# Optimization experiments

Measured on AMD Instinct MI355X. Metric: run time of the kernel, lower is better.

## Reference

```python
import jax, jax.numpy as jnp
import numpy as np

NORM_EPS = 1e-05

def _quant_input(x):
    # per-token dynamic int8 fake-quant: s = 127 / max(|x|, 1e-5)
    s = 127.0 / jnp.clip(jnp.max(jnp.abs(x), axis=-1, keepdims=True), 1e-05, None)
    return jnp.clip(jnp.round(x * s), -128.0, 127.0) / s

def _rmsnorm(x, w, eps):
    return x * jax.lax.rsqrt(jnp.mean(x * x, axis=-1, keepdims=True) + eps) * w

def setup_inputs() -> dict:
    key = jax.random.key(0)
    k0, k1, k2 = jax.random.split(key, 3)
    dim, hidden = 2048, 5632
    x = jax.random.normal(k0, (4, 2048, dim), dtype=jnp.float32)
    w13 = jax.random.normal(k1, (2 * hidden, dim), dtype=jnp.float32) * 0.02
    w2 = jax.random.normal(k2, (dim, hidden), dtype=jnp.float32) * 0.02
    norm_w = jnp.ones((hidden,), dtype=jnp.float32)
    return {"x": x, "w13": w13, "w2": w2, "norm_w": norm_w}

def reference(x, w13, w2, norm_w):
    # BitLinear w13: quantize input, then linear
    xq = _quant_input(x)
    x13 = jnp.einsum('bsd,fd->bsf', xq, w13)  # [B,S,2H]
    x1, x3 = jnp.split(x13, 2, axis=-1)
    gated = jnp.square(jax.nn.relu(x1)) * x3  # squared-ReLU gating
    inner = _rmsnorm(gated, norm_w, NORM_EPS)
    # BitLinear w2
    iq = _quant_input(inner)
    out = jnp.einsum('bsh,dh->bsd', iq, w2)
    return out
```

## Files before the change

### kernel.cpp

```cpp
#include <hip/hip_runtime.h>

typedef unsigned short u16;
typedef __attribute__((ext_vector_type(8))) short short8;
typedef __attribute__((ext_vector_type(4))) float f32x4;
typedef __attribute__((ext_vector_type(4))) u16 ushort4v;
typedef __attribute__((ext_vector_type(8))) u16 ushort8v;

#define DIM 2048
#define HID 5632
#define F2  11264
#define TTOT 8192

#define GLD(g, l) __builtin_amdgcn_global_load_lds(                       \
    (const __attribute__((address_space(1))) void*)(g),                   \
    (__attribute__((address_space(3))) void*)(l), 16, 0, 0)

__device__ __forceinline__ u16 f2bf(float f) {
  unsigned int u = __builtin_bit_cast(unsigned int, f);
  u += 0x7FFFu + ((u >> 16) & 1u);
  return (u16)(u >> 16);
}

__global__ __launch_bounds__(256) void conv_w13(const float* __restrict__ w,
                                                u16* __restrict__ o) {
  int idx = blockIdx.x * 256 + threadIdx.x;
  int rnew = idx >> 9;
  int dc = (idx & 511) << 2;
  int b = rnew >> 5, ii = rnew & 31;
  int orig = (ii < 16) ? (b * 16 + ii) : (HID + b * 16 + (ii - 16));
  float4 v = *reinterpret_cast<const float4*>(w + (size_t)orig * DIM + dc);
  ushort4v q = {f2bf(v.x), f2bf(v.y), f2bf(v.z), f2bf(v.w)};
  *reinterpret_cast<ushort4v*>(o + (size_t)rnew * DIM + dc) = q;
}

__global__ __launch_bounds__(256) void conv_w2(const float* __restrict__ w,
                                               u16* __restrict__ o) {
  size_t e = ((size_t)blockIdx.x * 256 + threadIdx.x) * 4;
  float4 v = *reinterpret_cast<const float4*>(w + e);
  ushort4v q = {f2bf(v.x), f2bf(v.y), f2bf(v.z), f2bf(v.w)};
  *reinterpret_cast<ushort4v*>(o + e) = q;
}

__global__ __launch_bounds__(256) void quant_x(const float* __restrict__ x,
                                               u16* __restrict__ q,
                                               float* __restrict__ scale) {
  const int t = blockIdx.x;
  const float* xr = x + (size_t)t * DIM;
  const int tid = threadIdx.x;
  float4 a = *reinterpret_cast<const float4*>(xr + tid * 8);
  float4 b = *reinterpret_cast<const float4*>(xr + tid * 8 + 4);
  float v[8] = {a.x, a.y, a.z, a.w, b.x, b.y, b.z, b.w};
  float m = 0.f;
#pragma unroll
  for (int i = 0; i < 8; ++i) m = fmaxf(m, fabsf(v[i]));
#pragma unroll
  for (int off = 32; off; off >>= 1) m = fmaxf(m, __shfl_xor(m, off));
  __shared__ float red[4];
  if ((tid & 63) == 0) red[tid >> 6] = m;
  __syncthreads();
  m = fmaxf(fmaxf(red[0], red[1]), fmaxf(red[2], red[3]));
  m = fmaxf(m, 1e-5f);
  float s = 127.0f / m;
  if (tid == 0) scale[t] = m / 127.0f;
  ushort8v o;
#pragma unroll
  for (int i = 0; i < 8; ++i) {
    float r = fminf(fmaxf(rintf(v[i] * s), -128.f), 127.f);
    o[i] = f2bf(r);
  }
  *reinterpret_cast<ushort8v*>(q + (size_t)t * DIM + tid * 8) = o;
}

__global__ __launch_bounds__(256) void gate_nq(const float* __restrict__ G,
                                               const float* __restrict__ nw,
                                               u16* __restrict__ q2,
                                               float* __restrict__ s2) {
  const int t = blockIdx.x;
  const float* gr = G + (size_t)t * HID;
  const int tid = threadIdx.x;
  float4 vv[6];
  float ss = 0.f, mx = 0.f;
#pragma unroll
  for (int k = 0; k < 6; ++k) {
    int i = tid + k * 256;
    if (i < 1408) {
      float4 v = *reinterpret_cast<const float4*>(gr + i * 4);
      float4 w4 = *reinterpret_cast<const float4*>(nw + i * 4);
      vv[k] = v;
      ss += v.x * v.x + v.y * v.y + v.z * v.z + v.w * v.w;
      mx = fmaxf(mx, fmaxf(fmaxf(fabsf(v.x * w4.x), fabsf(v.y * w4.y)),
                           fmaxf(fabsf(v.z * w4.z), fabsf(v.w * w4.w))));
    }
  }
#pragma unroll
  for (int off = 32; off; off >>= 1) {
    ss += __shfl_xor(ss, off);
    mx = fmaxf(mx, __shfl_xor(mx, off));
  }
  __shared__ float rs[4], rm[4];
  if ((tid & 63) == 0) { rs[tid >> 6] = ss; rm[tid >> 6] = mx; }
  __syncthreads();
  ss = rs[0] + rs[1] + rs[2] + rs[3];
  mx = fmaxf(fmaxf(rm[0], rm[1]), fmaxf(rm[2], rm[3]));
  float rinv = 1.0f / sqrtf(ss * (1.0f / 5632.0f) + 1e-5f);
  float mi = fmaxf(mx * rinv, 1e-5f);
  float s = 127.0f / mi;
  if (tid == 0) s2[t] = mi / 127.0f;
  float fs = rinv * s;
#pragma unroll
  for (int k = 0; k < 6; ++k) {
    int i = tid + k * 256;
    if (i < 1408) {
      float4 v = vv[k];
      float4 w4 = *reinterpret_cast<const float4*>(nw + i * 4);
      ushort4v o;
      o.x = f2bf(fminf(fmaxf(rintf(v.x * w4.x * fs), -128.f), 127.f));
      o.y = f2bf(fminf(fmaxf(rintf(v.y * w4.y * fs), -128.f), 127.f));
      o.z = f2bf(fminf(fmaxf(rintf(v.z * w4.z * fs), -128.f), 127.f));
      o.w = f2bf(fminf(fmaxf(rintf(v.w * w4.w * fs), -128.f), 127.f));
      *reinterpret_cast<ushort4v*>(q2 + (size_t)t * HID + i * 4) = o;
    }
  }
}

template <int GATE>
__global__ __launch_bounds__(512, 2) void gemm8(
    const u16* __restrict__ A, const u16* __restrict__ B,
    const float* __restrict__ rowscale, float* __restrict__ C,
    int N, int K, int Ntiles) {
  __shared__ __attribute__((aligned(16))) u16 lds[2][2][2][256 * 32];
  const int NT = K >> 6;
  const int nwg = gridDim.x;
  const int orig = blockIdx.x;
  const int qq = nwg >> 3, rr = nwg & 7, xcd = orig & 7, sidx = orig >> 3;
  const int wg = (xcd < rr ? xcd * (qq + 1) : rr * (qq + 1) + (xcd - rr) * qq) + sidx;
  const int mt = wg / Ntiles, nt = wg % Ntiles;

  const int tid = threadIdx.x;
  const int wid = tid >> 6, lane = tid & 63;
  const int wm = wid >> 2, wn = wid & 3;
  const int c16 = lane & 15, q4 = lane >> 4;
  const int rA_base = wm * 128 + c16;
  const int rB_base = wn * 64 + c16;
  const int caf = (q4 ^ ((lane >> 1) & 3)) << 3;

  const int sr = tid >> 2;
  const int scol = ((tid & 3) ^ ((tid >> 3) & 3)) << 3;
  const u16* Ar = A + ((size_t)mt * 256 + sr) * K + scol;
  const u16* Br = B + ((size_t)nt * 256 + sr) * K + scol;
  const size_t rstep = (size_t)128 * K;

  f32x4 acc[8][4];
#pragma unroll
  for (int m = 0; m < 8; ++m)
#pragma unroll
    for (int n = 0; n < 4; ++n) acc[m][n] = f32x4{0.f, 0.f, 0.f, 0.f};

  auto stage = [&](int mat, int kk, int t) {
    if (t < NT) {
      const u16* g = (mat ? Br : Ar) + t * 64 + kk * 32;
      u16* l = &lds[t & 1][mat][kk][wid << 9];
      GLD(g, l);
      GLD(g + rstep, l + 4096);
    }
  };
  auto ldA = [&](int db, int kk, int mh, short8* af) {
#pragma unroll
    for (int m = 0; m < 4; ++m)
      af[m] = *reinterpret_cast<const short8*>(
          &lds[db][0][kk][(rA_base + (mh * 4 + m) * 16) * 32 + caf]);
  };
  auto ldB = [&](int db, int kk, short8* bfr) {
#pragma unroll
    for (int n = 0; n < 4; ++n)
      bfr[n] = *reinterpret_cast<const short8*>(
          &lds[db][1][kk][(rB_base + n * 16) * 32 + caf]);
  };

  stage(1, 0, 0); stage(0, 0, 0); stage(1, 1, 0); stage(0, 1, 0);
  stage(1, 0, 1); stage(0, 0, 1); stage(1, 1, 1);
  asm volatile("s_waitcnt vmcnt(6)" ::: "memory");
  asm volatile("s_barrier" ::: "memory");

  for (int u = 0; u < NT; ++u) {
    const int db = u & 1;
    short8 af[4], bfr[4];
    ldB(db, 0, bfr);
    ldA(db, 0, 0, af);
    stage(0, 1, u + 1);
    asm volatile("s_barrier" ::: "memory");
    __builtin_amdgcn_s_setprio(1);
#pragma unroll
    for (int m = 0; m < 4; ++m)
#pragma unroll
      for (int n = 0; n < 4; ++n)
        acc[m][n] = __builtin_amdgcn_mfma_f32_16x16x32_bf16(af[m], bfr[n], acc[m][n], 0, 0, 0);
    __builtin_amdgcn_s_setprio(0);
    __builtin_amdgcn_sched_barrier(0);
    asm volatile("s_barrier" ::: "memory");
    ldA(db, 0, 1, af);
    stage(1, 0, u + 2);
    asm volatile("s_barrier" ::: "memory");
    __builtin_amdgcn_s_setprio(1);
#pragma unroll
    for (int m = 0; m < 4; ++m)
#pragma unroll
      for (int n = 0; n < 4; ++n)
        acc[4 + m][n] = __builtin_amdgcn_mfma_f32_16x16x32_bf16(af[m], bfr[n], acc[4 + m][n], 0, 0, 0);
    __builtin_amdgcn_s_setprio(0);
    __builtin_amdgcn_sched_barrier(0);
    asm volatile("s_barrier" ::: "memory");
    ldB(db, 1, bfr);
    ldA(db, 1, 0, af);
    stage(0, 0, u + 2);
    asm volatile("s_barrier" ::: "memory");
    __builtin_amdgcn_s_setprio(1);
#pragma unroll
    for (int m = 0; m < 4; ++m)
#pragma unroll
      for (int n = 0; n < 4; ++n)
        acc[m][n] = __builtin_amdgcn_mfma_f32_16x16x32_bf16(af[m], bfr[n], acc[m][n], 0, 0, 0);
    __builtin_amdgcn_s_setprio(0);
    __builtin_amdgcn_sched_barrier(0);
    asm volatile("s_barrier" ::: "memory");
    ldA(db, 1, 1, af);
    stage(1, 1, u + 2);
    if (u + 2 < NT) asm volatile("s_waitcnt vmcnt(6)" ::: "memory");
    else            asm volatile("s_waitcnt vmcnt(0)" ::: "memory");
    asm volatile("s_barrier" ::: "memory");
    __builtin_amdgcn_s_setprio(1);
#pragma unroll
    for (int m = 0; m < 4; ++m)
#pragma unroll
      for (int n = 0; n < 4; ++n)
        acc[4 + m][n] = __builtin_amdgcn_mfma_f32_16x16x32_bf16(af[m], bfr[n], acc[4 + m][n], 0, 0, 0);
    __builtin_amdgcn_s_setprio(0);
    __builtin_amdgcn_sched_barrier(0);
    asm volatile("s_barrier" ::: "memory");
  }

  const int mbase0 = mt * 256 + wm * 128;
  if constexpr (GATE == 0) {
#pragma unroll
    for (int m = 0; m < 8; ++m) {
#pragma unroll
      for (int j = 0; j < 4; ++j) {
        const int row = mbase0 + m * 16 + q4 * 4 + j;
        const float sc = rowscale[row];
        float* crow = C + (size_t)row * N + nt * 256 + wn * 64 + c16;
#pragma unroll
        for (int n = 0; n < 4; ++n) crow[n * 16] = acc[m][n][j] * sc;
      }
    }
  } else {
    const int H = N >> 1;
    const int gbase = (nt * 256 + wn * 64) >> 1;
#pragma unroll
    for (int m = 0; m < 8; ++m) {
#pragma unroll
      for (int j = 0; j < 4; ++j) {
        const int row = mbase0 + m * 16 + q4 * 4 + j;
        const float sc = rowscale[row];
        const float s3 = sc * sc * sc;
        float* grow = C + (size_t)row * H + gbase + c16;
#pragma unroll
        for (int p = 0; p < 2; ++p) {
          float a1 = acc[m][2 * p][j];
          float a3 = acc[m][2 * p + 1][j];
          float rl = fmaxf(a1, 0.f);
          grow[p * 16] = rl * rl * a3 * s3;
        }
      }
    }
  }
}

extern "C" void kernel_launch(void* const* d_in, const int* in_sizes, int n_in,
                              void* d_out, int out_size, void* d_ws, size_t ws_size,
                              hipStream_t stream) {
  const float* x = (const float*)d_in[0];
  const float* w13 = (const float*)d_in[1];
  const float* w2 = (const float*)d_in[2];
  const float* nw = (const float*)d_in[3];
  float* out = (float*)d_out;

  char* p = (char*)d_ws;
  u16* w13p = (u16*)p; p += (size_t)F2 * DIM * 2;
  u16* w2b = (u16*)p;  p += (size_t)DIM * HID * 2;
  u16* q2f = (u16*)p;  p += (size_t)TTOT * HID * 2;
  float* s2f = (float*)p; p += (size_t)TTOT * 4;
  const size_t fixed = (size_t)F2 * DIM * 2 + (size_t)DIM * HID * 2 +
                       (size_t)TTOT * HID * 2 + (size_t)TTOT * 4;
  const size_t perTok = (size_t)DIM * 2 + (size_t)HID * 4 + 8;
  int Tc = TTOT;
  while (Tc > 256 && fixed + (size_t)Tc * perTok > ws_size) Tc >>= 1;
  u16* q1 = (u16*)p;        p += (size_t)Tc * DIM * 2;
  float* gated = (float*)p; p += (size_t)Tc * HID * 4;
  float* s1 = (float*)p;

  conv_w13<<<F2 * DIM / 4 / 256, 256, 0, stream>>>(w13, w13p);
  conv_w2<<<DIM * HID / 4 / 256, 256, 0, stream>>>(w2, w2b);

  for (int t0 = 0; t0 < TTOT; t0 += Tc) {
    quant_x<<<Tc, 256, 0, stream>>>(x + (size_t)t0 * DIM, q1, s1);
    gemm8<1><<<(Tc / 256) * (F2 / 256), 512, 0, stream>>>(q1, w13p, s1, gated,
                                                          F2, DIM, F2 / 256);
    gate_nq<<<Tc, 256, 0, stream>>>(gated, nw, q2f + (size_t)t0 * HID, s2f + t0);
  }
  gemm8<0><<<(TTOT / 256) * (DIM / 256), 512, 0, stream>>>(q2f, w2b, s2f, out,
                                                           DIM, HID, DIM / 256);
}
```

Before: 630.1 us.

## Double-buffer MFMA fragment registers to overlap LDS reads with compute

```diff
diff --git a/kernel.cpp b/kernel.cpp
--- a/kernel.cpp
+++ b/kernel.cpp
@@ -177,65 +177,55 @@
           &lds[db][1][kk][(rB_base + n * 16) * 32 + caf]);
   };
 
+#define MFMA16(AF, BF, OFS)                                                   \
+  __builtin_amdgcn_s_setprio(1);                                              \
+  _Pragma("unroll") for (int m = 0; m < 4; ++m)                               \
+      _Pragma("unroll") for (int n = 0; n < 4; ++n)                           \
+          acc[(OFS) + m][n] = __builtin_amdgcn_mfma_f32_16x16x32_bf16(        \
+              AF[m], BF[n], acc[(OFS) + m][n], 0, 0, 0);                      \
+  __builtin_amdgcn_s_setprio(0);                                              \
+  __builtin_amdgcn_sched_barrier(0);
+
   stage(1, 0, 0); stage(0, 0, 0); stage(1, 1, 0); stage(0, 1, 0);
   stage(1, 0, 1); stage(0, 0, 1); stage(1, 1, 1);
   asm volatile("s_waitcnt vmcnt(6)" ::: "memory");
   asm volatile("s_barrier" ::: "memory");
 
+  short8 af_a[4], af_b[4], bf_a[4], bf_b[4];
+  ldB(0, 0, bf_a);
+  ldA(0, 0, 0, af_a);
+
   for (int u = 0; u < NT; ++u) {
     const int db = u & 1;
-    short8 af[4], bfr[4];
-    ldB(db, 0, bfr);
-    ldA(db, 0, 0, af);
     stage(0, 1, u + 1);
     asm volatile("s_barrier" ::: "memory");
-    __builtin_amdgcn_s_setprio(1);
-#pragma unroll
-    for (int m = 0; m < 4; ++m)
-#pragma unroll
-      for (int n = 0; n < 4; ++n)
-        acc[m][n] = __builtin_amdgcn_mfma_f32_16x16x32_bf16(af[m], bfr[n], acc[m][n], 0, 0, 0);
-    __builtin_amdgcn_s_setprio(0);
+    ldA(db, 0, 1, af_b);
     __builtin_amdgcn_sched_barrier(0);
-    asm volatile("s_barrier" ::: "memory");
-    ldA(db, 0, 1, af);
+    MFMA16(af_a, bf_a, 0)
+    asm volatile("s_barrier" ::: "memory");
     stage(1, 0, u + 2);
     asm volatile("s_barrier" ::: "memory");
-    __builtin_amdgcn_s_setprio(1);
-#pragma unroll
-    for (int m = 0; m < 4; ++m)
-#pragma unroll
-      for (int n = 0; n < 4; ++n)
-        acc[4 + m][n] = __builtin_amdgcn_mfma_f32_16x16x32_bf16(af[m], bfr[n], acc[4 + m][n], 0, 0, 0);
-    __builtin_amdgcn_s_setprio(0);
+    ldB(db, 1, bf_b);
+    ldA(db, 1, 0, af_a);
     __builtin_amdgcn_sched_barrier(0);
-    asm volatile("s_barrier" ::: "memory");
-    ldB(db, 1, bfr);
-    ldA(db, 1, 0, af);
+    MFMA16(af_b, bf_a, 4)
+    asm volatile("s_barrier" ::: "memory");
     stage(0, 0, u + 2);
     asm volatile("s_barrier" ::: "memory");
-    __builtin_amdgcn_s_setprio(1);
-#pragma unroll
-    for (int m = 0; m < 4; ++m)
-#pragma unroll
-      for (int n = 0; n < 4; ++n)
-        acc[m][n] = __builtin_amdgcn_mfma_f32_16x16x32_bf16(af[m], bfr[n], acc[m][n], 0, 0, 0);
-    __builtin_amdgcn_s_setprio(0);
+    ldA(db, 1, 1, af_b);
     __builtin_amdgcn_sched_barrier(0);
-    asm volatile("s_barrier" ::: "memory");
-    ldA(db, 1, 1, af);
+    MFMA16(af_a, bf_b, 0)
+    asm volatile("s_barrier" ::: "memory");
     stage(1, 1, u + 2);
     if (u + 2 < NT) asm volatile("s_waitcnt vmcnt(6)" ::: "memory");
     else            asm volatile("s_waitcnt vmcnt(0)" ::: "memory");
     asm volatile("s_barrier" ::: "memory");
-    __builtin_amdgcn_s_setprio(1);
-#pragma unroll
-    for (int m = 0; m < 4; ++m)
-#pragma unroll
-      for (int n = 0; n < 4; ++n)
-        acc[4 + m][n] = __builtin_amdgcn_mfma_f32_16x16x32_bf16(af[m], bfr[n], acc[4 + m][n], 0, 0, 0);
-    __builtin_amdgcn_s_setprio(0);
+    if (u + 1 < NT) {
+      ldB(db ^ 1, 0, bf_a);
+      ldA(db ^ 1, 0, 0, af_a);
+    }
     __builtin_amdgcn_sched_barrier(0);
+    MFMA16(af_b, bf_b, 4)
     asm volatile("s_barrier" ::: "memory");
   }
 
```

Measured after the change: 643.1 us. +2.1%, slower.
